# Kernel optimization log

Measured on AMD Instinct MI355X. Metric: run time of the kernel, lower is better.

The kernel has to match this reference:

```python
import jax, jax.numpy as jnp
import numpy as np

B, DIM_IN, DIM_OUT = 2048, 4096, 4096


def setup_inputs() -> dict:
    key = jax.random.key(0)
    k1, k2, k3 = jax.random.split(key, 3)
    # binary input activations (0/1), stored as int32
    x = jax.random.randint(k1, (B, DIM_IN), 0, 2, dtype=jnp.int32)
    masks = jax.random.uniform(k2, (DIM_IN, DIM_OUT)) < 0.5
    # integer thresholds in [0, dim_in)
    thresholds = jax.random.randint(k3, (DIM_OUT,), 0, DIM_IN, dtype=jnp.int32)
    return {"x": x, "masks": masks, "thresholds": thresholds}


def reference(x, masks, thresholds):
    # Original: expand x to (B, dim_in, dim_out), XNOR with masks, sum over dim_in,
    # compare vs thresholds. XNOR(a,b) = a*b + (1-a)*(1-b), so the sum over dim_in
    # is two GEMMs -- never materialize the (B, dim_in, dim_out) tensor.
    xf = x.astype(jnp.float32)              # (B, dim_in), values in {0,1}
    mf = masks.astype(jnp.float32)          # (dim_in, dim_out)
    sums = xf @ mf + (1.0 - xf) @ (1.0 - mf)  # (B, dim_out), popcount of agreements
    return sums > thresholds.astype(jnp.float32)[None, :]  # (B, dim_out) bool
```

## Files before the change

kernel.cpp:

```cpp
#include <hip/hip_runtime.h>
#include <stdint.h>

#define BB    2048
#define DIN   4096
#define DOUT  4096


using v4i  = __attribute__((ext_vector_type(4)))  int;
using v16i = __attribute__((ext_vector_type(16))) int;

__device__ __forceinline__ void async_load16(const void* g, void* l) {
    __builtin_amdgcn_global_load_lds(
        (const __attribute__((address_space(1))) unsigned int*)g,
        (__attribute__((address_space(3))) unsigned int*)l,
        16, 0, 0);
}

__device__ __forceinline__ unsigned int to_pm1(unsigned int c) {
    return c + ((c ^ 0x01010101u) * 255u);
}

__global__ void pack_all(const int* __restrict__ x,
                         const void* __restrict__ mraw,
                         char* __restrict__ x8,
                         char* __restrict__ m8T) {
    const int tid = threadIdx.x;
    if (blockIdx.x < BB) {
        const int row = blockIdx.x;
        const int4* src = (const int4*)(x + (size_t)row * DIN);
        unsigned int* dst = (unsigned int*)(x8 + (size_t)row * DIN);
        #pragma unroll
        for (int q = 0; q < 4; ++q) {
            int4 v = src[q * 256 + tid];
            unsigned int t = (unsigned int)(v.x & 1) |
                             ((unsigned int)(v.y & 1) << 8) |
                             ((unsigned int)(v.z & 1) << 16) |
                             ((unsigned int)(v.w & 1) << 24);
            dst[q * 256 + tid] = to_pm1(t);
        }
    } else {
        const int bw = blockIdx.x - BB;
        const int k0 = (bw & 63) * 64;
        const int n0 = (bw >> 6) * 64;

        const unsigned char* mb = (const unsigned char*)mraw;
        const unsigned int pv = *(const unsigned int*)(mb + (tid & 63) * 4);
        const bool isU8 = __any(pv > 1u);

        const int n4 = (tid & 15) * 4;
        const int k4 = (tid >> 4) * 4;
        unsigned int a[4];
        if (isU8) {
            #pragma unroll
            for (int r = 0; r < 4; ++r)
                a[r] = *(const unsigned int*)(mb + (size_t)(k0 + k4 + r) * DOUT + n0 + n4);
        } else {
            const int4* m32 = (const int4*)mraw;
            #pragma unroll
            for (int r = 0; r < 4; ++r) {
                int4 v = m32[((size_t)(k0 + k4 + r) * DOUT + n0 + n4) >> 2];
                a[r] = (unsigned int)(v.x & 1) |
                       ((unsigned int)(v.y & 1) << 8) |
                       ((unsigned int)(v.z & 1) << 16) |
                       ((unsigned int)(v.w & 1) << 24);
            }
        }
        unsigned int x0 = __builtin_amdgcn_perm(a[1], a[0], 0x05010400u);
        unsigned int x1 = __builtin_amdgcn_perm(a[3], a[2], 0x05010400u);
        unsigned int x2 = __builtin_amdgcn_perm(a[1], a[0], 0x07030602u);
        unsigned int x3 = __builtin_amdgcn_perm(a[3], a[2], 0x07030602u);
        unsigned int c0 = __builtin_amdgcn_perm(x1, x0, 0x05040100u);
        unsigned int c1 = __builtin_amdgcn_perm(x1, x0, 0x07060302u);
        unsigned int c2 = __builtin_amdgcn_perm(x3, x2, 0x05040100u);
        unsigned int c3 = __builtin_amdgcn_perm(x3, x2, 0x07060302u);
        *(unsigned int*)(m8T + (size_t)(n0 + n4 + 0) * DIN + k0 + k4) = to_pm1(c0);
        *(unsigned int*)(m8T + (size_t)(n0 + n4 + 1) * DIN + k0 + k4) = to_pm1(c1);
        *(unsigned int*)(m8T + (size_t)(n0 + n4 + 2) * DIN + k0 + k4) = to_pm1(c2);
        *(unsigned int*)(m8T + (size_t)(n0 + n4 + 3) * DIN + k0 + k4) = to_pm1(c3);
    }
}

__global__ __launch_bounds__(512)
void bgemm(const char* __restrict__ x8,
           const char* __restrict__ m8T,
           const int* __restrict__ thr,
           int* __restrict__ out) {
    const int flat = blockIdx.x;
    const int xcd  = flat & 7;
    const int idx  = flat >> 3;
    const int bm   = (xcd & 1) * 4 + (idx & 3);
    const int bn   = (xcd >> 1) * 8 + (idx >> 2);
    const int b0   = bm * 256;
    const int o0   = bn * 128;

    const int tid  = threadIdx.x;
    const int lane = tid & 63;
    const int wv   = tid >> 6;
    const int im   = wv & 1;
    const int in_  = (wv >> 1) & 1;
    const int kh   = wv >> 2;
    const int wm   = im * 128;
    const int wn   = in_ * 64;
    const int l31  = lane & 31;
    const int lh   = lane >> 5;
    const int rsw  = l31 & 7;

    __shared__ __align__(16) char lds[3 * 49152];

    auto stage = [&](int c, int buf) {
        char* bufA = lds + buf * 49152;
        char* bufB = bufA + 32768;
        const int k0 = c * 128;
        const int r8 = lane >> 3;
        const int sl = lane & 7;
        #pragma unroll
        for (int h = 0; h < 4; ++h) {
            const int r0  = wv * 32 + h * 8;
            const int row = r0 + r8;
            const int g   = sl ^ (row & 7);
            async_load16(x8 + (size_t)(b0 + row) * DIN + k0 + g * 16,
                         bufA + r0 * 128 + lane * 16);
        }
        #pragma unroll
        for (int h = 0; h < 2; ++h) {
            const int r0  = wv * 16 + h * 8;
            const int row = r0 + r8;
            const int g   = sl ^ (row & 7);
            async_load16(m8T + (size_t)(o0 + row) * DIN + k0 + g * 16,
                         bufB + r0 * 128 + lane * 16);
        }
    };

    v16i acc[4][2];
    #pragma unroll
    for (int t = 0; t < 4; ++t)
        #pragma unroll
        for (int u = 0; u < 2; ++u)
            acc[t][u] = (v16i)(0);

    stage(0, 0);
    stage(1, 1);

    for (int c = 0; c < 32; ++c) {
        if (c < 31) asm volatile("s_waitcnt vmcnt(6)" ::: "memory");
        else        asm volatile("s_waitcnt vmcnt(0)" ::: "memory");
        __builtin_amdgcn_s_barrier();
        if (c < 30) stage(c + 2, (c + 2) % 3);

        const char* bufA = lds + (c % 3) * 49152;
        const char* bufB = bufA + 32768;
        #pragma unroll
        for (int ks = 0; ks < 2; ++ks) {
            const int slot = (((kh * 4 + ks * 2 + lh) ^ rsw)) * 16;
            v4i aF[4], bF[2];
            #pragma unroll
            for (int t = 0; t < 4; ++t)
                aF[t] = *(const v4i*)&bufA[(wm + t * 32 + l31) * 128 + slot];
            #pragma unroll
            for (int u = 0; u < 2; ++u)
                bF[u] = *(const v4i*)&bufB[(wn + u * 32 + l31) * 128 + slot];
            #pragma unroll
            for (int t = 0; t < 4; ++t)
                #pragma unroll
                for (int u = 0; u < 2; ++u)
                    acc[t][u] = __builtin_amdgcn_mfma_i32_32x32x32_i8(
                        aF[t], bF[u], acc[t][u], 0, 0, 0);
        }
    }
    __syncthreads();

    int* pool = (int*)lds;
    const int p = wv & 3;
    {
        const int give0 = kh ? 0 : 2;
        const int bw_ = p * 8192 + (kh ? 0 : 1) * 4096;
        #pragma unroll
        for (int tt = 0; tt < 2; ++tt) {
            const int t = give0 + tt;
            #pragma unroll
            for (int u = 0; u < 2; ++u)
                #pragma unroll
                for (int r = 0; r < 16; ++r) {
                    const int rowl = (r & 3) + 8 * (r >> 2) + 4 * lh;
                    pool[bw_ + (tt * 32 + rowl) * 64 + u * 32 + l31] = acc[t][u][r];
                }
        }
    }
    __syncthreads();
    const int keep0 = kh ? 2 : 0;
    const int br_ = p * 8192 + kh * 4096;
    #pragma unroll
    for (int tt = 0; tt < 2; ++tt) {
        const int t = keep0 + tt;
        #pragma unroll
        for (int u = 0; u < 2; ++u)
            #pragma unroll
            for (int r = 0; r < 16; ++r) {
                const int rowl = (r & 3) + 8 * (r >> 2) + 4 * lh;
                acc[t][u][r] += pool[br_ + (tt * 32 + rowl) * 64 + u * 32 + l31];
            }
    }

    #pragma unroll
    for (int u = 0; u < 2; ++u) {
        const int o   = o0 + wn + u * 32 + l31;
        const int lim = 2 * thr[o] - DIN;
        #pragma unroll
        for (int tt = 0; tt < 2; ++tt) {
            const int t = keep0 + tt;
            #pragma unroll
            for (int r = 0; r < 16; ++r) {
                const int rowl = (r & 3) + 8 * (r >> 2) + 4 * lh;
                const int b    = b0 + wm + kh * 64 + tt * 32 + rowl;
                out[(size_t)b * DOUT + o] = (acc[t][u][r] > lim) ? 1 : 0;
            }
        }
    }
}

extern "C" void kernel_launch(void* const* d_in, const int* in_sizes, int n_in,
                              void* d_out, int out_size, void* d_ws, size_t ws_size,
                              hipStream_t stream) {
    const int* x          = (const int*)d_in[0];
    const void* masks     = d_in[1];
    const int* thresholds = (const int*)d_in[2];
    int* out              = (int*)d_out;

    char* x8  = (char*)d_ws;
    char* m8T = (char*)d_ws + ((size_t)8 << 20);

    pack_all<<<BB + 4096, 256, 0, stream>>>(x, masks, x8, m8T);
    bgemm<<<256, 512, 0, stream>>>(x8, m8T, thresholds, out);
}
```

Before: 174.6 us.

## Shrink GEMM tile to 128x128, double-buffer with barriers, and transpose masks via LDS

The mask pack kernel now handles 64x256 tiles and transposes through shared memory, so it does wide 16-byte coalesced writes to the transposed int8 mask. The GEMM kernel moves from 256x128 tiles with 8 waves and a triple-buffered async pipeline to 128x128 tiles with 4 waves, 512 blocks and a simpler double buffer synchronised by __syncthreads each step. s_setprio is raised around the MFMA bursts. This aims for more blocks per CU and better pack bandwidth, at the cost of less reuse per tile and a full barrier every k-step.

```diff
diff --git a/kernel.cpp b/kernel.cpp
--- a/kernel.cpp
+++ b/kernel.cpp
@@ -40,47 +40,68 @@
         }
     } else {
         const int bw = blockIdx.x - BB;
-        const int k0 = (bw & 63) * 64;
-        const int n0 = (bw >> 6) * 64;
+        const int n0 = (bw >> 4) * 64;
+        const int k0 = (bw & 15) * 256;
+
+        __shared__ unsigned int tl[64][68];
 
         const unsigned char* mb = (const unsigned char*)mraw;
         const unsigned int pv = *(const unsigned int*)(mb + (tid & 63) * 4);
         const bool isU8 = __any(pv > 1u);
 
-        const int n4 = (tid & 15) * 4;
-        const int k4 = (tid >> 4) * 4;
-        unsigned int a[4];
+        const int kq4  = tid >> 2;
+        const int nq16 = (tid & 3) * 16;
+        unsigned int b[4][4];
         if (isU8) {
             #pragma unroll
-            for (int r = 0; r < 4; ++r)
-                a[r] = *(const unsigned int*)(mb + (size_t)(k0 + k4 + r) * DOUT + n0 + n4);
+            for (int r = 0; r < 4; ++r) {
+                uint4 v = *(const uint4*)(mb + (size_t)(k0 + kq4 * 4 + r) * DOUT
+                                          + n0 + nq16);
+                b[r][0] = v.x; b[r][1] = v.y; b[r][2] = v.z; b[r][3] = v.w;
+            }
         } else {
             const int4* m32 = (const int4*)mraw;
             #pragma unroll
-            for (int r = 0; r < 4; ++r) {
-                int4 v = m32[((size_t)(k0 + k4 + r) * DOUT + n0 + n4) >> 2];
-                a[r] = (unsigned int)(v.x & 1) |
-                       ((unsigned int)(v.y & 1) << 8) |
-                       ((unsigned int)(v.z & 1) << 16) |
-                       ((unsigned int)(v.w & 1) << 24);
-            }
-        }
-        unsigned int x0 = __builtin_amdgcn_perm(a[1], a[0], 0x05010400u);
-        unsigned int x1 = __builtin_amdgcn_perm(a[3], a[2], 0x05010400u);
-        unsigned int x2 = __builtin_amdgcn_perm(a[1], a[0], 0x07030602u);
-        unsigned int x3 = __builtin_amdgcn_perm(a[3], a[2], 0x07030602u);
-        unsigned int c0 = __builtin_amdgcn_perm(x1, x0, 0x05040100u);
-        unsigned int c1 = __builtin_amdgcn_perm(x1, x0, 0x07060302u);
-        unsigned int c2 = __builtin_amdgcn_perm(x3, x2, 0x05040100u);
-        unsigned int c3 = __builtin_amdgcn_perm(x3, x2, 0x07060302u);
-        *(unsigned int*)(m8T + (size_t)(n0 + n4 + 0) * DIN + k0 + k4) = to_pm1(c0);
-        *(unsigned int*)(m8T + (size_t)(n0 + n4 + 1) * DIN + k0 + k4) = to_pm1(c1);
-        *(unsigned int*)(m8T + (size_t)(n0 + n4 + 2) * DIN + k0 + k4) = to_pm1(c2);
-        *(unsigned int*)(m8T + (size_t)(n0 + n4 + 3) * DIN + k0 + k4) = to_pm1(c3);
-    }
-}
-
-__global__ __launch_bounds__(512)
+            for (int r = 0; r < 4; ++r)
+                #pragma unroll
+                for (int q = 0; q < 4; ++q) {
+                    int4 v = m32[((size_t)(k0 + kq4 * 4 + r) * DOUT
+                                  + n0 + nq16 + q * 4) >> 2];
+                    b[r][q] = (unsigned int)(v.x & 1) |
+                              ((unsigned int)(v.y & 1) << 8) |
+                              ((unsigned int)(v.z & 1) << 16) |
+                              ((unsigned int)(v.w & 1) << 24);
+                }
+        }
+        #pragma unroll
+        for (int w = 0; w < 4; ++w) {
+            unsigned int a0 = b[0][w], a1 = b[1][w], a2 = b[2][w], a3 = b[3][w];
+            unsigned int x0 = __builtin_amdgcn_perm(a1, a0, 0x05010400u);
+            unsigned int x1 = __builtin_amdgcn_perm(a3, a2, 0x05010400u);
+            unsigned int x2 = __builtin_amdgcn_perm(a1, a0, 0x07030602u);
+            unsigned int x3 = __builtin_amdgcn_perm(a3, a2, 0x07030602u);
+            unsigned int c0 = __builtin_amdgcn_perm(x1, x0, 0x05040100u);
+            unsigned int c1 = __builtin_amdgcn_perm(x1, x0, 0x07060302u);
+            unsigned int c2 = __builtin_amdgcn_perm(x3, x2, 0x05040100u);
+            unsigned int c3 = __builtin_amdgcn_perm(x3, x2, 0x07060302u);
+            tl[nq16 + w * 4 + 0][kq4] = to_pm1(c0);
+            tl[nq16 + w * 4 + 1][kq4] = to_pm1(c1);
+            tl[nq16 + w * 4 + 2][kq4] = to_pm1(c2);
+            tl[nq16 + w * 4 + 3][kq4] = to_pm1(c3);
+        }
+        __syncthreads();
+
+        const int nr = tid >> 2;
+        const int c4 = tid & 3;
+        #pragma unroll
+        for (int q = 0; q < 4; ++q) {
+            uint4 v = *(const uint4*)&tl[nr][4 * (c4 + 4 * q)];
+            *(uint4*)(m8T + (size_t)(n0 + nr) * DIN + k0 + 16 * (c4 + 4 * q)) = v;
+        }
+    }
+}
+
+__global__ __launch_bounds__(256)
 void bgemm(const char* __restrict__ x8,
            const char* __restrict__ m8T,
            const int* __restrict__ thr,
@@ -88,28 +109,26 @@
     const int flat = blockIdx.x;
     const int xcd  = flat & 7;
     const int idx  = flat >> 3;
-    const int bm   = (xcd & 1) * 4 + (idx & 3);
-    const int bn   = (xcd >> 1) * 8 + (idx >> 2);
-    const int b0   = bm * 256;
+    const int bm   = (xcd & 1) * 8 + (idx & 7);
+    const int bn   = (xcd >> 1) * 8 + (idx >> 3);
+    const int b0   = bm * 128;
     const int o0   = bn * 128;
 
     const int tid  = threadIdx.x;
     const int lane = tid & 63;
     const int wv   = tid >> 6;
-    const int im   = wv & 1;
-    const int in_  = (wv >> 1) & 1;
-    const int kh   = wv >> 2;
-    const int wm   = im * 128;
+    const int in_  = wv & 1;
+    const int kh   = wv >> 1;
     const int wn   = in_ * 64;
     const int l31  = lane & 31;
     const int lh   = lane >> 5;
     const int rsw  = l31 & 7;
 
-    __shared__ __align__(16) char lds[3 * 49152];
+    __shared__ __align__(16) char lds[65536];
 
     auto stage = [&](int c, int buf) {
-        char* bufA = lds + buf * 49152;
-        char* bufB = bufA + 32768;
+        char* bufA = lds + buf * 32768;
+        char* bufB = bufA + 16384;
         const int k0 = c * 128;
         const int r8 = lane >> 3;
         const int sl = lane & 7;
@@ -120,12 +139,6 @@
             const int g   = sl ^ (row & 7);
             async_load16(x8 + (size_t)(b0 + row) * DIN + k0 + g * 16,
                          bufA + r0 * 128 + lane * 16);
-        }
-        #pragma unroll
-        for (int h = 0; h < 2; ++h) {
-            const int r0  = wv * 16 + h * 8;
-            const int row = r0 + r8;
-            const int g   = sl ^ (row & 7);
             async_load16(m8T + (size_t)(o0 + row) * DIN + k0 + g * 16,
                          bufB + r0 * 128 + lane * 16);
         }
@@ -139,38 +152,38 @@
             acc[t][u] = (v16i)(0);
 
     stage(0, 0);
-    stage(1, 1);
+    __syncthreads();
 
     for (int c = 0; c < 32; ++c) {
-        if (c < 31) asm volatile("s_waitcnt vmcnt(6)" ::: "memory");
-        else        asm volatile("s_waitcnt vmcnt(0)" ::: "memory");
-        __builtin_amdgcn_s_barrier();
-        if (c < 30) stage(c + 2, (c + 2) % 3);
-
-        const char* bufA = lds + (c % 3) * 49152;
-        const char* bufB = bufA + 32768;
+        const int buf = c & 1;
+        if (c < 31) stage(c + 1, buf ^ 1);
+
+        const char* bufA = lds + buf * 32768;
+        const char* bufB = bufA + 16384;
         #pragma unroll
         for (int ks = 0; ks < 2; ++ks) {
             const int slot = (((kh * 4 + ks * 2 + lh) ^ rsw)) * 16;
             v4i aF[4], bF[2];
             #pragma unroll
             for (int t = 0; t < 4; ++t)
-                aF[t] = *(const v4i*)&bufA[(wm + t * 32 + l31) * 128 + slot];
+                aF[t] = *(const v4i*)&bufA[(t * 32 + l31) * 128 + slot];
             #pragma unroll
             for (int u = 0; u < 2; ++u)
                 bF[u] = *(const v4i*)&bufB[(wn + u * 32 + l31) * 128 + slot];
+            __builtin_amdgcn_s_setprio(1);
             #pragma unroll
             for (int t = 0; t < 4; ++t)
                 #pragma unroll
                 for (int u = 0; u < 2; ++u)
                     acc[t][u] = __builtin_amdgcn_mfma_i32_32x32x32_i8(
                         aF[t], bF[u], acc[t][u], 0, 0, 0);
-        }
-    }
-    __syncthreads();
+            __builtin_amdgcn_s_setprio(0);
+        }
+        __syncthreads();
+    }
 
     int* pool = (int*)lds;
-    const int p = wv & 3;
+    const int p = in_;
     {
         const int give0 = kh ? 0 : 2;
         const int bw_ = p * 8192 + (kh ? 0 : 1) * 4096;
@@ -211,7 +224,7 @@
             #pragma unroll
             for (int r = 0; r < 16; ++r) {
                 const int rowl = (r & 3) + 8 * (r >> 2) + 4 * lh;
-                const int b    = b0 + wm + kh * 64 + tt * 32 + rowl;
+                const int b    = b0 + kh * 64 + tt * 32 + rowl;
                 out[(size_t)b * DOUT + o] = (acc[t][u][r] > lim) ? 1 : 0;
             }
         }
@@ -229,6 +242,6 @@
     char* x8  = (char*)d_ws;
     char* m8T = (char*)d_ws + ((size_t)8 << 20);
 
-    pack_all<<<BB + 4096, 256, 0, stream>>>(x, masks, x8, m8T);
-    bgemm<<<256, 512, 0, stream>>>(x8, m8T, thresholds, out);
-}
+    pack_all<<<BB + 1024, 256, 0, stream>>>(x, masks, x8, m8T);
+    bgemm<<<512, 256, 0, stream>>>(x8, m8T, thresholds, out);
+}
```

Measured after the change: 181.6 us. 4.0% more time.
